# Kernel tuning notes

Hardware: AMD Instinct MI355X
Metric: run time of the kernel (lower is better)

## Reference

```python
import jax, jax.numpy as jnp
import numpy as np

VOCAB = 50257
DIM = 1024
B, S = 4, 4096


def setup_inputs() -> dict:
    key = jax.random.key(0)
    k1, k2, k3 = jax.random.split(key, 3)
    input_ids = jax.random.randint(k1, (B, S), 0, VOCAB)
    weight = jax.random.normal(k2, (VOCAB, DIM), dtype=jnp.float32)
    # R initialized as a random matrix stand-in for the learned Stiefel rotation
    R = jax.random.normal(k3, (DIM, DIM), dtype=jnp.float32) / np.sqrt(DIM)
    return {"input_ids": input_ids, "weight": weight, "R": R}


def reference(input_ids, weight, R):
    # Faithful to the module: rotate the FULL embedding table, then gather.
    w_eff = weight @ R              # [V, D] @ [D, D] -> [V, D]
    return jnp.take(w_eff, input_ids, axis=0)  # [B, S, D]
```

## Files before the change

### kernel.cpp

```cpp
#include <hip/hip_runtime.h>
#include <hip/hip_bf16.h>


typedef __attribute__((ext_vector_type(4))) float f32x4;
typedef __attribute__((ext_vector_type(8))) short s16x8;
typedef __attribute__((ext_vector_type(2))) int i32x2;

#define DIM 1024
#define BKT 32
#define NT 32
#define BUF_SH (256 * BKT)

__device__ __forceinline__ short f2bf(float f) {
  unsigned u = __float_as_uint(f);
  unsigned r = (u + 0x7FFFu + ((u >> 16) & 1u)) >> 16;
  return (short)r;
}

__device__ __forceinline__ void gload_lds16(const void* g, void* l) {
  __builtin_amdgcn_global_load_lds((const __attribute__((address_space(1))) void*)g,
                                   (__attribute__((address_space(3))) void*)l, 16, 0, 0);
}

__global__ __launch_bounds__(256) void prep_kernel(const float* __restrict__ R,
                                                   short* __restrict__ RT,
                                                   const float* __restrict__ W,
                                                   const int* __restrict__ ids,
                                                   short* __restrict__ G) {
  const int b = blockIdx.x;
  const int t = threadIdx.x;
  if (b < 1024) {
    __shared__ float tile[32][33];
    const int bx = b & 31, by = b >> 5;
    const int tx = t & 31, ty = t >> 5;
#pragma unroll
    for (int i = 0; i < 4; ++i)
      tile[ty + i * 8][tx] = R[(size_t)(by * 32 + ty + i * 8) * DIM + bx * 32 + tx];
    __syncthreads();
#pragma unroll
    for (int i = 0; i < 4; ++i)
      RT[(size_t)(bx * 32 + ty + i * 8) * DIM + by * 32 + tx] = f2bf(tile[tx][ty + i * 8]);
  } else {
    const int tid = (b - 1024) * 256 + t;
#pragma unroll
    for (int i = 0; i < 8; ++i) {
      const int g = tid + i * (2048 * 256);
      const int row = g >> 8;
      const int c4 = (g & 255) << 2;
      const f32x4 v = *(const f32x4*)(W + (size_t)ids[row] * DIM + c4);
      i32x2 p;
      p[0] = (int)(unsigned short)f2bf(v[0]) | ((int)f2bf(v[1]) << 16);
      p[1] = (int)(unsigned short)f2bf(v[2]) | ((int)f2bf(v[3]) << 16);
      *(i32x2*)(G + (size_t)g * 4) = p;
    }
  }
}

__global__ __launch_bounds__(512, 2) void rot_embed_gemm(const short* __restrict__ G,
                                                         const short* __restrict__ RT,
                                                         float* __restrict__ out) {
  extern __shared__ char smem[];

  const int t = threadIdx.x;
  const int b = blockIdx.x;
  const int swz = (b & 7) * 32 + (b >> 3);
  const int m0 = (swz >> 2) * 256;
  const int n0 = (swz & 3) * 256;

  const int lane = t & 63;
  const int w = t >> 6;
  const int wm = w >> 2;
  const int wn = w & 3;
  const int fr = lane & 15;
  const int fq = lane >> 4;

  const int srow = w * 16 + (lane >> 2);
  const int schunk = ((lane & 3) ^ ((lane >> 2) & 3)) * 8;
  const short* gA0 = G + (size_t)(m0 + srow) * DIM + schunk;
  const short* gA1 = G + (size_t)(m0 + 128 + srow) * DIM + schunk;
  const short* gB0 = RT + (size_t)(n0 + srow) * DIM + schunk;
  const short* gB1 = RT + (size_t)(n0 + 128 + srow) * DIM + schunk;

  char* const ldsA = smem;
  char* const ldsB = smem + 3 * 32768 / 2;

#define STAGE(kt, d)                                             \
  {                                                              \
    const int ko = (kt) * BKT;                                   \
    char* la = ldsA + (d) * 16384 + w * 1024;                    \
    char* lb = ldsB + (d) * 16384 + w * 1024;                    \
    gload_lds16(gA0 + ko, la);                                   \
    gload_lds16(gA1 + ko, la + 8192);                            \
    gload_lds16(gB0 + ko, lb);                                   \
    gload_lds16(gB1 + ko, lb + 8192);                            \
  }

  f32x4 acc[8][4];
#pragma unroll
  for (int i = 0; i < 8; ++i)
#pragma unroll
    for (int j = 0; j < 4; ++j) acc[i][j] = (f32x4)0.0f;

  STAGE(0, 0);
  STAGE(1, 1);

  for (int kt = 0; kt < NT; ++kt) {
    if (kt == NT - 1)
      asm volatile("s_waitcnt vmcnt(0)" ::: "memory");
    else
      asm volatile("s_waitcnt vmcnt(4)" ::: "memory");
    __builtin_amdgcn_s_barrier();
    __builtin_amdgcn_sched_barrier(0);

    if (kt + 2 < NT) STAGE(kt + 2, (kt + 2) % 3);

    const char* A = ldsA + (kt % 3) * 16384;
    const char* B = ldsB + (kt % 3) * 16384;

    const int sc = (fq ^ (fr & 3)) << 4;
    s16x8 af[8], bf[4];
#pragma unroll
    for (int mi = 0; mi < 8; ++mi)
      af[mi] = *(const s16x8*)(A + (wm * 128 + mi * 16 + fr) * 64 + sc);
#pragma unroll
    for (int nj = 0; nj < 4; ++nj)
      bf[nj] = *(const s16x8*)(B + (wn * 64 + nj * 16 + fr) * 64 + sc);

    __builtin_amdgcn_s_setprio(1);
#pragma unroll
    for (int mi = 0; mi < 8; ++mi)
#pragma unroll
      for (int nj = 0; nj < 4; ++nj)
        acc[mi][nj] = __builtin_amdgcn_mfma_f32_16x16x32_bf16(af[mi], bf[nj], acc[mi][nj], 0, 0, 0);
    __builtin_amdgcn_s_setprio(0);
  }

#pragma unroll
  for (int mi = 0; mi < 8; ++mi)
#pragma unroll
    for (int nj = 0; nj < 4; ++nj) {
      float* op = out + (size_t)(m0 + wm * 128 + mi * 16 + fq * 4) * DIM +
                  (n0 + wn * 64 + nj * 16 + fr);
#pragma unroll
      for (int r = 0; r < 4; ++r) op[(size_t)r * DIM] = acc[mi][nj][r];
    }
#undef STAGE
}

extern "C" void kernel_launch(void* const* d_in, const int* in_sizes, int n_in,
                              void* d_out, int out_size, void* d_ws, size_t ws_size,
                              hipStream_t stream) {
  const int* ids = (const int*)d_in[0];
  const float* W = (const float*)d_in[1];
  const float* R = (const float*)d_in[2];
  float* out = (float*)d_out;
  short* RT = (short*)d_ws;
  short* G = (short*)d_ws + (size_t)DIM * DIM;

  prep_kernel<<<dim3(3072), dim3(256), 0, stream>>>(R, RT, W, ids, G);
  rot_embed_gemm<<<dim3(256), dim3(512), 98304, stream>>>(G, RT, out);
}
```

Measured before the change: 60.85 us.

## Fuse embedding gather and bf16 conversion into GEMM A-operand load

The separate prep pass that gathered weight rows by token id and wrote a bf16 copy to workspace is removed. The GEMM now loads fp32 rows of W directly through registers, converts them to bf16, and writes them into swizzled LDS, while B still streams via direct-to-LDS loads. The goal is to avoid the round trip of the gathered 16Kx1024 matrix through global memory and one kernel's worth of work. In exchange, A now takes a register-staged path with fp32 loads (twice the bytes), and the pipeline is hand-scheduled with a two-step unroll and explicit waitcnts.

Measured after the change: 70.42 us. 1.16x slower.

```diff
diff --git a/kernel.cpp b/kernel.cpp
--- a/kernel.cpp
+++ b/kernel.cpp
@@ -4,12 +4,9 @@
 
 typedef __attribute__((ext_vector_type(4))) float f32x4;
 typedef __attribute__((ext_vector_type(8))) short s16x8;
-typedef __attribute__((ext_vector_type(2))) int i32x2;
 
 #define DIM 1024
-#define BKT 32
 #define NT 32
-#define BUF_SH (256 * BKT)
 
 __device__ __forceinline__ short f2bf(float f) {
   unsigned u = __float_as_uint(f);
@@ -22,42 +19,23 @@
                                    (__attribute__((address_space(3))) void*)l, 16, 0, 0);
 }
 
-__global__ __launch_bounds__(256) void prep_kernel(const float* __restrict__ R,
-                                                   short* __restrict__ RT,
-                                                   const float* __restrict__ W,
-                                                   const int* __restrict__ ids,
-                                                   short* __restrict__ G) {
-  const int b = blockIdx.x;
-  const int t = threadIdx.x;
-  if (b < 1024) {
-    __shared__ float tile[32][33];
-    const int bx = b & 31, by = b >> 5;
-    const int tx = t & 31, ty = t >> 5;
+__global__ __launch_bounds__(256) void convert_R_kernel(const float* __restrict__ R,
+                                                        short* __restrict__ RT) {
+  __shared__ float tile[32][33];
+  const int bx = blockIdx.x, by = blockIdx.y;
+  const int tx = threadIdx.x, ty = threadIdx.y;
 #pragma unroll
-    for (int i = 0; i < 4; ++i)
-      tile[ty + i * 8][tx] = R[(size_t)(by * 32 + ty + i * 8) * DIM + bx * 32 + tx];
-    __syncthreads();
+  for (int i = 0; i < 4; ++i)
+    tile[ty + i * 8][tx] = R[(size_t)(by * 32 + ty + i * 8) * DIM + bx * 32 + tx];
+  __syncthreads();
 #pragma unroll
-    for (int i = 0; i < 4; ++i)
-      RT[(size_t)(bx * 32 + ty + i * 8) * DIM + by * 32 + tx] = f2bf(tile[tx][ty + i * 8]);
-  } else {
-    const int tid = (b - 1024) * 256 + t;
-#pragma unroll
-    for (int i = 0; i < 8; ++i) {
-      const int g = tid + i * (2048 * 256);
-      const int row = g >> 8;
-      const int c4 = (g & 255) << 2;
-      const f32x4 v = *(const f32x4*)(W + (size_t)ids[row] * DIM + c4);
-      i32x2 p;
-      p[0] = (int)(unsigned short)f2bf(v[0]) | ((int)f2bf(v[1]) << 16);
-      p[1] = (int)(unsigned short)f2bf(v[2]) | ((int)f2bf(v[3]) << 16);
-      *(i32x2*)(G + (size_t)g * 4) = p;
-    }
-  }
+  for (int i = 0; i < 4; ++i)
+    RT[(size_t)(bx * 32 + ty + i * 8) * DIM + by * 32 + tx] = f2bf(tile[tx][ty + i * 8]);
 }
 
-__global__ __launch_bounds__(512, 2) void rot_embed_gemm(const short* __restrict__ G,
+__global__ __launch_bounds__(512, 2) void rot_embed_gemm(const float* __restrict__ W,
                                                          const short* __restrict__ RT,
+                                                         const int* __restrict__ ids,
                                                          float* __restrict__ out) {
   extern __shared__ char smem[];
 
@@ -67,32 +45,65 @@
   const int m0 = (swz >> 2) * 256;
   const int n0 = (swz & 3) * 256;
 
+  int* sIds = (int*)(smem + 98304);
+  if (t < 256) sIds[t] = ids[m0 + t];
+  __syncthreads();
+
   const int lane = t & 63;
   const int w = t >> 6;
-  const int wm = w >> 2;
-  const int wn = w & 3;
-  const int fr = lane & 15;
-  const int fq = lane >> 4;
+  const int wm = w >> 2, wn = w & 3;
+  const int fr = lane & 15, fq = lane >> 4;
+
+  char* const ldsA = smem;
+  char* const ldsB = smem + 49152;
 
   const int srow = w * 16 + (lane >> 2);
   const int schunk = ((lane & 3) ^ ((lane >> 2) & 3)) * 8;
-  const short* gA0 = G + (size_t)(m0 + srow) * DIM + schunk;
-  const short* gA1 = G + (size_t)(m0 + 128 + srow) * DIM + schunk;
   const short* gB0 = RT + (size_t)(n0 + srow) * DIM + schunk;
   const short* gB1 = RT + (size_t)(n0 + 128 + srow) * DIM + schunk;
 
-  char* const ldsA = smem;
-  char* const ldsB = smem + 3 * 32768 / 2;
+  const int rA = t >> 1;
+  const int h = t & 1;
+  const float* gA = W + (size_t)sIds[rA] * DIM + h * 16;
+  const int wo0 = rA * 64 + (((h * 2) ^ (rA & 3)) << 4);
+  const int wo1 = rA * 64 + (((h * 2 + 1) ^ (rA & 3)) << 4);
 
-#define STAGE(kt, d)                                             \
-  {                                                              \
-    const int ko = (kt) * BKT;                                   \
-    char* la = ldsA + (d) * 16384 + w * 1024;                    \
-    char* lb = ldsB + (d) * 16384 + w * 1024;                    \
-    gload_lds16(gA0 + ko, la);                                   \
-    gload_lds16(gA1 + ko, la + 8192);                            \
-    gload_lds16(gB0 + ko, lb);                                   \
-    gload_lds16(gB1 + ko, lb + 8192);                            \
+#define ALD(av, kt)                                  \
+  {                                                  \
+    const f32x4* p = (const f32x4*)(gA + (kt) * 32); \
+    av[0] = p[0]; av[1] = p[1]; av[2] = p[2]; av[3] = p[3]; \
+  }
+#define BST(off, kt)                                                  \
+  {                                                                   \
+    gload_lds16(gB0 + (kt) * 32, ldsB + (off) + w * 1024);            \
+    gload_lds16(gB1 + (kt) * 32, ldsB + (off) + w * 1024 + 8192);     \
+  }
+#define AWR(av, off)                                                  \
+  {                                                                   \
+    s16x8 p0, p1;                                                     \
+    _Pragma("unroll") for (int e = 0; e < 4; ++e) {                   \
+      p0[e] = f2bf(av[0][e]); p0[4 + e] = f2bf(av[1][e]);             \
+      p1[e] = f2bf(av[2][e]); p1[4 + e] = f2bf(av[3][e]);             \
+    }                                                                 \
+    *(s16x8*)(ldsA + (off) + wo0) = p0;                               \
+    *(s16x8*)(ldsA + (off) + wo1) = p1;                               \
+  }
+#define COMPUTE(off)                                                         \
+  {                                                                          \
+    const char* Abuf = ldsA + (off);                                         \
+    const char* Bbuf = ldsB + (off);                                         \
+    const int sc = (fq ^ (fr & 3)) << 4;                                     \
+    s16x8 af[8], bfv[4];                                                     \
+    _Pragma("unroll") for (int mi = 0; mi < 8; ++mi)                         \
+        af[mi] = *(const s16x8*)(Abuf + (wm * 128 + mi * 16 + fr) * 64 + sc);\
+    _Pragma("unroll") for (int nj = 0; nj < 4; ++nj)                         \
+        bfv[nj] = *(const s16x8*)(Bbuf + (wn * 64 + nj * 16 + fr) * 64 + sc);\
+    __builtin_amdgcn_s_setprio(1);                                           \
+    _Pragma("unroll") for (int mi = 0; mi < 8; ++mi)                         \
+        _Pragma("unroll") for (int nj = 0; nj < 4; ++nj)                     \
+            acc[mi][nj] = __builtin_amdgcn_mfma_f32_16x16x32_bf16(           \
+                af[mi], bfv[nj], acc[mi][nj], 0, 0, 0);                      \
+    __builtin_amdgcn_s_setprio(0);                                           \
   }
 
   f32x4 acc[8][4];
@@ -101,38 +112,53 @@
 #pragma unroll
     for (int j = 0; j < 4; ++j) acc[i][j] = (f32x4)0.0f;
 
-  STAGE(0, 0);
-  STAGE(1, 1);
+  f32x4 avE[4], avO[4];
 
-  for (int kt = 0; kt < NT; ++kt) {
-    if (kt == NT - 1)
+  ALD(avE, 0);
+  __builtin_amdgcn_sched_barrier(0);
+  BST(0, 0);
+  __builtin_amdgcn_sched_barrier(0);
+  ALD(avO, 1);
+  __builtin_amdgcn_sched_barrier(0);
+  BST(16384, 1);
+  __builtin_amdgcn_sched_barrier(0);
+  asm volatile("s_waitcnt vmcnt(8)" ::: "memory");
+  AWR(avE, 0);
+  __builtin_amdgcn_sched_barrier(0);
+  asm volatile("s_waitcnt vmcnt(6) lgkmcnt(0)" ::: "memory");
+  __builtin_amdgcn_s_barrier();
+  __builtin_amdgcn_sched_barrier(0);
+
+  int offR = 0, offW = 16384, offS = 32768;
+
+  for (int kt = 0; kt < NT; kt += 2) {
+    if (kt + 2 < NT) { BST(offS, kt + 2); ALD(avE, kt + 2); }
+    __builtin_amdgcn_sched_barrier(0);
+    if (kt + 2 < NT)
+      asm volatile("s_waitcnt vmcnt(6)" ::: "memory");
+    else
       asm volatile("s_waitcnt vmcnt(0)" ::: "memory");
-    else
-      asm volatile("s_waitcnt vmcnt(4)" ::: "memory");
+    __builtin_amdgcn_sched_barrier(0);
+    AWR(avO, offW);
+    COMPUTE(offR);
+    asm volatile("s_waitcnt lgkmcnt(0)" ::: "memory");
     __builtin_amdgcn_s_barrier();
     __builtin_amdgcn_sched_barrier(0);
+    { const int tmp = offR; offR = offW; offW = offS; offS = tmp; }
 
-    if (kt + 2 < NT) STAGE(kt + 2, (kt + 2) % 3);
-
-    const char* A = ldsA + (kt % 3) * 16384;
-    const char* B = ldsB + (kt % 3) * 16384;
-
-    const int sc = (fq ^ (fr & 3)) << 4;
-    s16x8 af[8], bf[4];
-#pragma unroll
-    for (int mi = 0; mi < 8; ++mi)
-      af[mi] = *(const s16x8*)(A + (wm * 128 + mi * 16 + fr) * 64 + sc);
-#pragma unroll
-    for (int nj = 0; nj < 4; ++nj)
-      bf[nj] = *(const s16x8*)(B + (wn * 64 + nj * 16 + fr) * 64 + sc);
-
-    __builtin_amdgcn_s_setprio(1);
-#pragma unroll
-    for (int mi = 0; mi < 8; ++mi)
-#pragma unroll
-      for (int nj = 0; nj < 4; ++nj)
-        acc[mi][nj] = __builtin_amdgcn_mfma_f32_16x16x32_bf16(af[mi], bf[nj], acc[mi][nj], 0, 0, 0);
-    __builtin_amdgcn_s_setprio(0);
+    if (kt + 3 < NT) { BST(offS, kt + 3); ALD(avO, kt + 3); }
+    __builtin_amdgcn_sched_barrier(0);
+    if (kt + 3 < NT)
+      asm volatile("s_waitcnt vmcnt(6)" ::: "memory");
+    else
+      asm volatile("s_waitcnt vmcnt(0)" ::: "memory");
+    __builtin_amdgcn_sched_barrier(0);
+    if (kt + 2 < NT) AWR(avE, offW);
+    COMPUTE(offR);
+    asm volatile("s_waitcnt lgkmcnt(0)" ::: "memory");
+    __builtin_amdgcn_s_barrier();
+    __builtin_amdgcn_sched_barrier(0);
+    { const int tmp = offR; offR = offW; offW = offS; offS = tmp; }
   }
 
 #pragma unroll
@@ -144,7 +170,10 @@
 #pragma unroll
       for (int r = 0; r < 4; ++r) op[(size_t)r * DIM] = acc[mi][nj][r];
     }
-#undef STAGE
+#undef ALD
+#undef BST
+#undef AWR
+#undef COMPUTE
 }
 
 extern "C" void kernel_launch(void* const* d_in, const int* in_sizes, int n_in,
@@ -155,8 +184,7 @@
   const float* R = (const float*)d_in[2];
   float* out = (float*)d_out;
   short* RT = (short*)d_ws;
-  short* G = (short*)d_ws + (size_t)DIM * DIM;
 
-  prep_kernel<<<dim3(3072), dim3(256), 0, stream>>>(R, RT, W, ids, G);
-  rot_embed_gemm<<<dim3(256), dim3(512), 98304, stream>>>(G, RT, out);
+  convert_R_kernel<<<dim3(32, 32), dim3(32, 8), 0, stream>>>(R, RT);
+  rot_embed_gemm<<<dim3(256), dim3(512), 99328, stream>>>(W, RT, ids, out);
 }
```

## Double K-tile depth and split A/B staging into triple and double buffers

Applied to the files above, without the earlier changes.

The GEMM K-step grows from 32 to 64, halving the number of main-loop iterations and barriers. A tiles are now triple-buffered and B tiles double-buffered, with a new XOR swizzle for the wider 128-byte LDS rows. Each iteration runs two MFMA sub-steps over the wider tile. LDS use rises to 160 KB per block, which removes any chance of two resident blocks per CU and adds an explicit lgkmcnt wait before each barrier.

Result: faster. 57.42 us (-5.6%).

```diff
diff --git a/kernel.cpp b/kernel.cpp
--- a/kernel.cpp
+++ b/kernel.cpp
@@ -7,9 +7,7 @@
 typedef __attribute__((ext_vector_type(2))) int i32x2;
 
 #define DIM 1024
-#define BKT 32
-#define NT 32
-#define BUF_SH (256 * BKT)
+#define NT 16
 
 __device__ __forceinline__ short f2bf(float f) {
   unsigned u = __float_as_uint(f);
@@ -69,30 +67,29 @@
 
   const int lane = t & 63;
   const int w = t >> 6;
-  const int wm = w >> 2;
-  const int wn = w & 3;
-  const int fr = lane & 15;
-  const int fq = lane >> 4;
-
-  const int srow = w * 16 + (lane >> 2);
-  const int schunk = ((lane & 3) ^ ((lane >> 2) & 3)) * 8;
-  const short* gA0 = G + (size_t)(m0 + srow) * DIM + schunk;
-  const short* gA1 = G + (size_t)(m0 + 128 + srow) * DIM + schunk;
-  const short* gB0 = RT + (size_t)(n0 + srow) * DIM + schunk;
-  const short* gB1 = RT + (size_t)(n0 + 128 + srow) * DIM + schunk;
+  const int wm = w >> 2, wn = w & 3;
+  const int fr = lane & 15, fq = lane >> 4;
 
   char* const ldsA = smem;
-  char* const ldsB = smem + 3 * 32768 / 2;
+  char* const ldsB = smem + 98304;
 
-#define STAGE(kt, d)                                             \
-  {                                                              \
-    const int ko = (kt) * BKT;                                   \
-    char* la = ldsA + (d) * 16384 + w * 1024;                    \
-    char* lb = ldsB + (d) * 16384 + w * 1024;                    \
-    gload_lds16(gA0 + ko, la);                                   \
-    gload_lds16(gA1 + ko, la + 8192);                            \
-    gload_lds16(gB0 + ko, lb);                                   \
-    gload_lds16(gB1 + ko, lb + 8192);                            \
+  const int srow = w * 8 + (lane >> 3);
+  const int sch = ((lane & 7) ^ (lane >> 3)) * 8;
+  const short* gA = G + (size_t)(m0 + srow) * DIM + sch;
+  const short* gB = RT + (size_t)(n0 + srow) * DIM + sch;
+  const int ldsOff = w * 1024;
+
+#define STA(buf, kt)                                                        \
+  {                                                                         \
+    _Pragma("unroll") for (int j = 0; j < 4; ++j)                           \
+        gload_lds16(gA + (size_t)j * 64 * DIM + (kt) * 64,                  \
+                    ldsA + (buf) * 32768 + j * 8192 + ldsOff);              \
+  }
+#define STB(buf, kt)                                                        \
+  {                                                                         \
+    _Pragma("unroll") for (int j = 0; j < 4; ++j)                           \
+        gload_lds16(gB + (size_t)j * 64 * DIM + (kt) * 64,                  \
+                    ldsB + (buf) * 32768 + j * 8192 + ldsOff);              \
   }
 
   f32x4 acc[8][4];
@@ -101,38 +98,45 @@
 #pragma unroll
     for (int j = 0; j < 4; ++j) acc[i][j] = (f32x4)0.0f;
 
-  STAGE(0, 0);
-  STAGE(1, 1);
+  STA(0, 0);
+  STB(0, 0);
+  STA(1, 1);
 
+  int bA = 0, bB = 0;
   for (int kt = 0; kt < NT; ++kt) {
     if (kt == NT - 1)
       asm volatile("s_waitcnt vmcnt(0)" ::: "memory");
     else
       asm volatile("s_waitcnt vmcnt(4)" ::: "memory");
+    asm volatile("s_waitcnt lgkmcnt(0)" ::: "memory");
     __builtin_amdgcn_s_barrier();
-    __builtin_amdgcn_sched_barrier(0);
 
-    if (kt + 2 < NT) STAGE(kt + 2, (kt + 2) % 3);
+    if (kt + 1 < NT) STB(bB ^ 1, kt + 1);
+    if (kt + 2 < NT) { const int nb = (bA + 2 >= 3) ? bA - 1 : bA + 2; STA(nb, kt + 2); }
 
-    const char* A = ldsA + (kt % 3) * 16384;
-    const char* B = ldsB + (kt % 3) * 16384;
-
-    const int sc = (fq ^ (fr & 3)) << 4;
-    s16x8 af[8], bf[4];
+    const char* A = ldsA + bA * 32768;
+    const char* B = ldsB + bB * 32768;
 #pragma unroll
-    for (int mi = 0; mi < 8; ++mi)
-      af[mi] = *(const s16x8*)(A + (wm * 128 + mi * 16 + fr) * 64 + sc);
+    for (int kk = 0; kk < 2; ++kk) {
+      const int sl = ((fq + 4 * kk) ^ (fr & 7)) << 4;
+      s16x8 af[8], bfv[4];
 #pragma unroll
-    for (int nj = 0; nj < 4; ++nj)
-      bf[nj] = *(const s16x8*)(B + (wn * 64 + nj * 16 + fr) * 64 + sc);
-
-    __builtin_amdgcn_s_setprio(1);
-#pragma unroll
-    for (int mi = 0; mi < 8; ++mi)
+      for (int mi = 0; mi < 8; ++mi)
+        af[mi] = *(const s16x8*)(A + (wm * 128 + mi * 16 + fr) * 128 + sl);
 #pragma unroll
       for (int nj = 0; nj < 4; ++nj)
-        acc[mi][nj] = __builtin_amdgcn_mfma_f32_16x16x32_bf16(af[mi], bf[nj], acc[mi][nj], 0, 0, 0);
-    __builtin_amdgcn_s_setprio(0);
+        bfv[nj] = *(const s16x8*)(B + (wn * 64 + nj * 16 + fr) * 128 + sl);
+      __builtin_amdgcn_s_setprio(1);
+#pragma unroll
+      for (int mi = 0; mi < 8; ++mi)
+#pragma unroll
+        for (int nj = 0; nj < 4; ++nj)
+          acc[mi][nj] = __builtin_amdgcn_mfma_f32_16x16x32_bf16(af[mi], bfv[nj], acc[mi][nj], 0, 0, 0);
+      __builtin_amdgcn_s_setprio(0);
+    }
+
+    bA = (bA + 1 == 3) ? 0 : bA + 1;
+    bB ^= 1;
   }
 
 #pragma unroll
@@ -144,7 +148,8 @@
 #pragma unroll
       for (int r = 0; r < 4; ++r) op[(size_t)r * DIM] = acc[mi][nj][r];
     }
-#undef STAGE
+#undef STA
+#undef STB
 }
 
 extern "C" void kernel_launch(void* const* d_in, const int* in_sizes, int n_in,
@@ -158,5 +163,5 @@
   short* G = (short*)d_ws + (size_t)DIM * DIM;
 
   prep_kernel<<<dim3(3072), dim3(256), 0, stream>>>(R, RT, W, ids, G);
-  rot_embed_gemm<<<dim3(256), dim3(512), 98304, stream>>>(G, RT, out);
+  rot_embed_gemm<<<dim3(256), dim3(512), 163840, stream>>>(G, RT, out);
 }
```
